# Kernel optimization log

Hardware: AMD Instinct MI355X
Metric: run time of the kernel (lower is better)

## Reference

```python
import jax, jax.numpy as jnp
import numpy as np

B, T, E, H = 4, 4096, 512, 64

def setup_inputs() -> dict:
    key = jax.random.key(0)
    k1, k2, k3, k4 = jax.random.split(key, 4)
    x = jax.random.normal(k1, (B, T, E), dtype=jnp.float32)
    # nn.Linear(E, H, bias=False) weight has shape [H, E]; y = x @ W.T
    Wq = jax.random.normal(k2, (H, E), dtype=jnp.float32) * (E ** -0.5)
    Wk = jax.random.normal(k3, (H, E), dtype=jnp.float32) * (E ** -0.5)
    Wv = jax.random.normal(k4, (H, E), dtype=jnp.float32) * (E ** -0.5)
    return {"x": x, "Wq": Wq, "Wk": Wk, "Wv": Wv}

def reference(x, Wq, Wk, Wv):
    # projections: [B, T, H]
    q = jnp.einsum('bte,he->bth', x, Wq)
    k = jnp.einsum('bte,he->bth', x, Wk)
    v = jnp.einsum('bte,he->bth', x, Wv)
    scale = 1.0 / jnp.sqrt(jnp.float32(q.shape[-1]))
    scores = jnp.einsum('bth,bsh->bts', q, k) * scale  # [B, T, T]
    t = scores.shape[-1]
    causal = jnp.tril(jnp.ones((t, t), dtype=bool))
    scores = jnp.where(causal, scores, -jnp.inf)
    probs = jax.nn.softmax(scores, axis=-1)
    # dropout p=0.0 (eval) -> identity
    return jnp.einsum('bts,bsh->bth', probs, v)
```

## Files before the change

kernel.cpp:

```cpp
#include <hip/hip_runtime.h>
#include <hip/hip_bf16.h>

#define Bn 4
#define Tn 4096
#define En 512
#define Hn 64
#define NEGINF -3e38f
#define QSCALE 0.1803368801f

typedef __attribute__((ext_vector_type(8))) __bf16 bf16x8;
typedef __attribute__((ext_vector_type(4))) __bf16 bf16x4;
typedef __attribute__((ext_vector_type(4))) float f32x4;

#define MFMA16(a, b, c) __builtin_amdgcn_mfma_f32_16x16x32_bf16(a, b, c, 0, 0, 0)

__device__ __forceinline__ float bf2f(unsigned short u) {
    union { unsigned u; float f; } v; v.u = ((unsigned)u) << 16;
    return v.f;
}
__device__ __forceinline__ unsigned cvtpk(float a, float b) {
    unsigned d;
    asm("v_cvt_pk_bf16_f32 %0, %1, %2" : "=v"(d) : "v"(a), "v"(b));
    return d;
}
__device__ __forceinline__ unsigned short f2bf(float f) {
    union { float f; unsigned u; } v; v.f = f;
    unsigned r = v.u + 0x7fffu + ((v.u >> 16) & 1u);
    return (unsigned short)(r >> 16);
}
__device__ __forceinline__ float exp2fast(float x) {
    float r;
    asm("v_exp_f32 %0, %1" : "=v"(r) : "v"(x));
    return r;
}
__device__ __forceinline__ void gl16(const void* g, void* l) {
    __builtin_amdgcn_global_load_lds(
        (const __attribute__((address_space(1))) unsigned int*)g,
        (__attribute__((address_space(3))) unsigned int*)l, 16, 0, 0);
}

__launch_bounds__(256, 2)
__global__ void proj(const float* __restrict__ x, const float* __restrict__ Wq,
                     const float* __restrict__ Wk, const float* __restrict__ Wv,
                     unsigned short* __restrict__ q16, unsigned short* __restrict__ k16,
                     unsigned short* __restrict__ vt16) {
    __shared__ __align__(16) unsigned char plds[2][28672];
    const int tid = threadIdx.x;
    const int w = tid >> 6, lane = tid & 63, r = lane & 15, g = lane >> 4;
    const int row0 = blockIdx.x * 32;
    const int rsel = (w & 1) * 16, csel = (w >> 1) * 96;

    const int srow = tid >> 3, skc = (tid & 7) * 8;
    const int sby = (tid & 7) * 16;

    f32x4 acc[6];
#pragma unroll
    for (int i = 0; i < 6; ++i) acc[i] = (f32x4){0.f, 0.f, 0.f, 0.f};

    {
        const float4* xp = (const float4*)&x[(row0 + srow) * En + skc];
        float4 f0 = xp[0], f1 = xp[1];
        union { bf16x8 v; unsigned u32[4]; } t;
        t.u32[0] = cvtpk(f0.x, f0.y); t.u32[1] = cvtpk(f0.z, f0.w);
        t.u32[2] = cvtpk(f1.x, f1.y); t.u32[3] = cvtpk(f1.z, f1.w);
        *(bf16x8*)&plds[0][srow * 128 + (sby ^ ((srow & 7) << 4))] = t.v;
#pragma unroll
        for (int c2 = 0; c2 < 6; ++c2) {
            const float* Ws = (c2 < 2) ? Wq : ((c2 < 4) ? Wk : Wv);
            int wr = (c2 & 1) * 32 + srow;
            const float4* wp = (const float4*)&Ws[wr * En + skc];
            float4 w0 = wp[0], w1 = wp[1];
            union { bf16x8 v; unsigned u32[4]; } tw;
            tw.u32[0] = cvtpk(w0.x, w0.y); tw.u32[1] = cvtpk(w0.z, w0.w);
            tw.u32[2] = cvtpk(w1.x, w1.y); tw.u32[3] = cvtpk(w1.z, w1.w);
            int wrow = c2 * 32 + srow;
            *(bf16x8*)&plds[0][4096 + wrow * 128 + (sby ^ ((wrow & 7) << 4))] = tw.v;
        }
    }
    __syncthreads();

    for (int s = 0; s < 8; ++s) {
        const int pp = s & 1;
        const bool more = (s < 7);
        float4 nf0, nf1;
        float4 nw0[6], nw1[6];
        if (more) {
            int k1 = (s + 1) * 64;
            const float4* xp = (const float4*)&x[(row0 + srow) * En + k1 + skc];
            nf0 = xp[0]; nf1 = xp[1];
#pragma unroll
            for (int c2 = 0; c2 < 6; ++c2) {
                const float* Ws = (c2 < 2) ? Wq : ((c2 < 4) ? Wk : Wv);
                int wr = (c2 & 1) * 32 + srow;
                const float4* wp = (const float4*)&Ws[wr * En + k1 + skc];
                nw0[c2] = wp[0]; nw1[c2] = wp[1];
            }
        }
        {
            const unsigned char* A = &plds[pp][0];
            const unsigned char* W = &plds[pp][4096];
            int arow = rsel + r, asw = (arow & 7) << 4;
            bf16x8 a0 = *(const bf16x8*)&A[arow * 128 + ((g * 16) ^ asw)];
            bf16x8 a1 = *(const bf16x8*)&A[arow * 128 + ((64 + g * 16) ^ asw)];
#pragma unroll
            for (int ct = 0; ct < 6; ++ct) {
                int wrow = csel + ct * 16 + r, wsw = (wrow & 7) << 4;
                bf16x8 b0 = *(const bf16x8*)&W[wrow * 128 + ((g * 16) ^ wsw)];
                bf16x8 b1 = *(const bf16x8*)&W[wrow * 128 + ((64 + g * 16) ^ wsw)];
                acc[ct] = MFMA16(a0, b0, acc[ct]);
                acc[ct] = MFMA16(a1, b1, acc[ct]);
            }
        }
        if (more) {
            unsigned char* D = &plds[pp ^ 1][0];
            union { bf16x8 v; unsigned u32[4]; } t;
            t.u32[0] = cvtpk(nf0.x, nf0.y); t.u32[1] = cvtpk(nf0.z, nf0.w);
            t.u32[2] = cvtpk(nf1.x, nf1.y); t.u32[3] = cvtpk(nf1.z, nf1.w);
            *(bf16x8*)&D[srow * 128 + (sby ^ ((srow & 7) << 4))] = t.v;
#pragma unroll
            for (int c2 = 0; c2 < 6; ++c2) {
                union { bf16x8 v; unsigned u32[4]; } tw;
                tw.u32[0] = cvtpk(nw0[c2].x, nw0[c2].y); tw.u32[1] = cvtpk(nw0[c2].z, nw0[c2].w);
                tw.u32[2] = cvtpk(nw1[c2].x, nw1[c2].y); tw.u32[3] = cvtpk(nw1[c2].z, nw1[c2].w);
                int wrow = c2 * 32 + srow;
                *(bf16x8*)&D[4096 + wrow * 128 + (sby ^ ((wrow & 7) << 4))] = tw.v;
            }
        }
        __syncthreads();
    }
#pragma unroll
    for (int ct = 0; ct < 6; ++ct) {
        int n = csel + ct * 16 + r;
#pragma unroll
        for (int reg = 0; reg < 4; ++reg) {
            int gr = row0 + rsel + g * 4 + reg;
            if (n < 64) {
                q16[gr * 64 + n] = f2bf(acc[ct][reg] * QSCALE);
            } else if (n < 128) {
                k16[gr * 64 + (n - 64)] = f2bf(acc[ct][reg]);
            } else {
                int h = n - 128; int bb = gr >> 12; int t = gr & 4095;
                vt16[((bb * 64 + h) << 12) + t] = f2bf(acc[ct][reg]);
            }
        }
    }
}

__launch_bounds__(256, 5)
__global__ void attnp(const unsigned short* __restrict__ q16, const unsigned short* __restrict__ k16,
                      const unsigned short* __restrict__ vt16,
                      unsigned short* __restrict__ po, float* __restrict__ lp) {
    __shared__ __align__(16) unsigned char lds[2][16384];

    const int tid = threadIdx.x;
    const int w = tid >> 6, lane = tid & 63, r = lane & 15, g = lane >> 4;
    const int bid = blockIdx.x;
    const int page = bid >> 8, idx = bid & 255;
    const int s5 = idx >> 3, b = (idx >> 1) & 3, q1 = idx & 1;
    int jt, piece, t0, tEnd;
    if (page < 3) {
        jt = 63 - s5;
        int nt = jt + 1;
        piece = page + 3 * q1;
        t0 = (piece * nt) / 6; tEnd = ((piece + 1) * nt) / 6;
    } else {
        jt = s5;
        int nt = jt + 1;
        piece = (page - 3) + 2 * q1;
        t0 = (piece * nt) / 4; tEnd = ((piece + 1) * nt) / 4;
    }
    const size_t kbase = (size_t)b * Tn;
    const int q0 = jt * 64;
    const int wq0 = q0 + w * 16;

    const unsigned short* Kb = k16 + kbase * 64;
    const unsigned short* Vb = vt16 + ((size_t)(b * 64) << 12);

    const int srl = lane >> 3, scb = (lane & 7) * 16;

    bf16x8 bq0, bq1;
    {
        const unsigned short* qp = &q16[(kbase + wq0 + r) * 64 + g * 8];
        bq0 = *(const bf16x8*)qp;
        bq1 = *(const bf16x8*)(qp + 32);
    }

    f32x4 o[4];
#pragma unroll
    for (int i = 0; i < 4; ++i) o[i] = (f32x4){0.f, 0.f, 0.f, 0.f};
    float l_ = 0.f;

    if (tEnd > t0) {
        int kv0 = t0 * 64;
#pragma unroll
        for (int i = 0; i < 4; ++i) {
            int cc = w * 4 + i;
            if (cc < 8) {
                int row = cc * 8 + srl, sw = (row & 7) << 4;
                gl16((const char*)Kb + (size_t)(kv0 + row) * 128 + (scb ^ sw),
                     &lds[0][cc * 1024]);
            } else {
                int h = (cc - 8) * 8 + srl, sw = (h & 7) << 4;
                gl16((const char*)Vb + (size_t)h * 8192 + (size_t)kv0 * 2 + (scb ^ sw),
                     &lds[0][cc * 1024]);
            }
        }
    }
    __syncthreads();

    int pp = 0;
    for (int it = t0; it < tEnd; ++it, pp ^= 1) {
        const bool more = (it + 1 < tEnd);
        if (more) {
            int nkv = (it + 1) * 64;
#pragma unroll
            for (int i = 0; i < 4; ++i) {
                int cc = w * 4 + i;
                if (cc < 8) {
                    int row = cc * 8 + srl, sw = (row & 7) << 4;
                    gl16((const char*)Kb + (size_t)(nkv + row) * 128 + (scb ^ sw),
                         &lds[pp ^ 1][cc * 1024]);
                } else {
                    int h = (cc - 8) * 8 + srl, sw = (h & 7) << 4;
                    gl16((const char*)Vb + (size_t)h * 8192 + (size_t)nkv * 2 + (scb ^ sw),
                         &lds[pp ^ 1][cc * 1024]);
                }
            }
        }
        const int kv0 = it * 64;
        if (kv0 <= wq0 + 15) {
            const unsigned char* K = &lds[pp][0];
            const unsigned char* V = &lds[pp][8192];
            f32x4 s4[4];
            __builtin_amdgcn_s_setprio(1);
#pragma unroll
            for (int ct = 0; ct < 4; ++ct) {
                int row = ct * 16 + r;
                int base = row * 128, sw = (row & 7) << 4;
                bf16x8 ak0 = *(const bf16x8*)&K[base + ((g * 16) ^ sw)];
                bf16x8 ak1 = *(const bf16x8*)&K[base + ((64 + g * 16) ^ sw)];
                f32x4 t = (f32x4){0.f, 0.f, 0.f, 0.f};
                t = MFMA16(ak0, bq0, t);
                t = MFMA16(ak1, bq1, t);
                s4[ct] = t;
            }
            __builtin_amdgcn_s_setprio(0);
            if (kv0 + 63 > wq0) {
                int qq = wq0 + r;
#pragma unroll
                for (int ct = 0; ct < 4; ++ct)
#pragma unroll
                    for (int reg = 0; reg < 4; ++reg) {
                        int kv = kv0 + ct * 16 + g * 4 + reg;
                        if (kv > qq) s4[ct][reg] = NEGINF;
                    }
            }
#pragma unroll
            for (int ct = 0; ct < 4; ++ct)
#pragma unroll
                for (int reg = 0; reg < 4; ++reg)
                    s4[ct][reg] = exp2fast(s4[ct][reg]);
            l_ += ((s4[0][0] + s4[0][1]) + (s4[0][2] + s4[0][3])) +
                  ((s4[1][0] + s4[1][1]) + (s4[1][2] + s4[1][3])) +
                  ((s4[2][0] + s4[2][1]) + (s4[2][2] + s4[2][3])) +
                  ((s4[3][0] + s4[3][1]) + (s4[3][2] + s4[3][3]));
            union { bf16x8 v; unsigned u32[4]; } pk[2];
#pragma unroll
            for (int kf = 0; kf < 2; ++kf) {
                pk[kf].u32[0] = cvtpk(s4[kf * 2][0], s4[kf * 2][1]);
                pk[kf].u32[1] = cvtpk(s4[kf * 2][2], s4[kf * 2][3]);
                pk[kf].u32[2] = cvtpk(s4[kf * 2 + 1][0], s4[kf * 2 + 1][1]);
                pk[kf].u32[3] = cvtpk(s4[kf * 2 + 1][2], s4[kf * 2 + 1][3]);
            }
            __builtin_amdgcn_s_setprio(1);
#pragma unroll
            for (int cth = 0; cth < 4; ++cth) {
                int h = cth * 16 + r;
                int vb = h * 128, sw2 = (h & 7) << 4;
#pragma unroll
                for (int kf = 0; kf < 2; ++kf) {
                    int off = kf * 64 + g * 8;
                    union { bf16x8 v; bf16x4 h4[2]; } vv;
                    vv.h4[0] = *(const bf16x4*)&V[vb + (off ^ sw2)];
                    vv.h4[1] = *(const bf16x4*)&V[vb + ((off + 32) ^ sw2)];
                    o[cth] = MFMA16(pk[kf].v, vv.v, o[cth]);
                }
            }
            __builtin_amdgcn_s_setprio(0);
        }
        __syncthreads();
    }

    const size_t qb = (size_t)piece * 16384 + b * 4096;
#pragma unroll
    for (int cth = 0; cth < 4; ++cth)
#pragma unroll
        for (int reg = 0; reg < 4; ++reg)
            po[(qb + wq0 + g * 4 + reg) * 64 + cth * 16 + r] = f2bf(o[cth][reg]);
    lp[(qb + wq0 + r) * 4 + g] = l_;
}

__global__ void merge(const unsigned short* __restrict__ po, const float* __restrict__ lp,
                      float* __restrict__ out) {
    int t = blockIdx.x * 256 + threadIdx.x;
    int q = t >> 3, c8 = (t & 7) * 8;
    int tloc = (q & 4095) >> 6;
    int ns = (tloc >= 32) ? 6 : 4;
    float L = 0.f;
    for (int c = 0; c < ns; ++c)
#pragma unroll
        for (int gg = 0; gg < 4; ++gg)
            L += lp[((size_t)c * 16384 + q) * 4 + gg];
    float inv = 1.0f / L;
    float acc[8] = {0.f, 0.f, 0.f, 0.f, 0.f, 0.f, 0.f, 0.f};
    for (int c = 0; c < ns; ++c) {
        union { uint4 v; unsigned short u[8]; } ld;
        ld.v = *(const uint4*)&po[((size_t)c * 16384 + q) * 64 + c8];
#pragma unroll
        for (int j = 0; j < 8; ++j) acc[j] += bf2f(ld.u[j]);
    }
    float4* op = (float4*)&out[(size_t)q * 64 + c8];
    op[0] = (float4){acc[0] * inv, acc[1] * inv, acc[2] * inv, acc[3] * inv};
    op[1] = (float4){acc[4] * inv, acc[5] * inv, acc[6] * inv, acc[7] * inv};
}

extern "C" void kernel_launch(void* const* d_in, const int* in_sizes, int n_in,
                              void* d_out, int out_size, void* d_ws, size_t ws_size,
                              hipStream_t stream) {
    const float* x  = (const float*)d_in[0];
    const float* Wq = (const float*)d_in[1];
    const float* Wk = (const float*)d_in[2];
    const float* Wv = (const float*)d_in[3];
    float* out = (float*)d_out;
    char* ws = (char*)d_ws;

    unsigned short* q16 = (unsigned short*)ws;
    unsigned short* k16 = (unsigned short*)(ws + 2097152);
    unsigned short* v16 = (unsigned short*)(ws + 4194304);
    unsigned short* po  = (unsigned short*)(ws + 6291456);
    float*          lp  = (float*)(ws + 18874368);

    hipLaunchKernelGGL(proj, dim3(512), dim3(256), 0, stream, x, Wq, Wk, Wv, q16, k16, v16);
    hipLaunchKernelGGL(attnp, dim3(1280), dim3(256), 0, stream, q16, k16, v16, po, lp);
    hipLaunchKernelGGL(merge, dim3(512), dim3(256), 0, stream, po, lp, out);
}
```

Before: 46.76 us.

## Split every query tile into four KV chunks and use one barrier per iteration

The attention work split changes from a mixed 6-way/4-way scheme (1280 blocks) to a uniform 4-way split over KV tiles (1024 blocks), pairing long and short query tiles by block index. The merge kernel then always combines four partials with unrolled loops. The pipeline drops the trailing __syncthreads and instead waits on vmcnt and issues one barrier at the top of each iteration, with buffer parity taken from the tile index. Launch bounds drop from 5 to 4 waves per SIMD. This may trade load balance across CUs for less merge work and fewer synchronisations.

```diff
diff --git a/kernel.cpp b/kernel.cpp
--- a/kernel.cpp
+++ b/kernel.cpp
@@ -146,7 +146,7 @@
     }
 }
 
-__launch_bounds__(256, 5)
+__launch_bounds__(256, 4)
 __global__ void attnp(const unsigned short* __restrict__ q16, const unsigned short* __restrict__ k16,
                       const unsigned short* __restrict__ vt16,
                       unsigned short* __restrict__ po, float* __restrict__ lp) {
@@ -155,22 +155,15 @@
     const int tid = threadIdx.x;
     const int w = tid >> 6, lane = tid & 63, r = lane & 15, g = lane >> 4;
     const int bid = blockIdx.x;
-    const int page = bid >> 8, idx = bid & 255;
+    const int k_ = bid >> 8, idx = bid & 255;
     const int s5 = idx >> 3, b = (idx >> 1) & 3, q1 = idx & 1;
-    int jt, piece, t0, tEnd;
-    if (page < 3) {
-        jt = 63 - s5;
-        int nt = jt + 1;
-        piece = page + 3 * q1;
-        t0 = (piece * nt) / 6; tEnd = ((piece + 1) * nt) / 6;
-    } else {
-        jt = s5;
-        int nt = jt + 1;
-        piece = (page - 3) + 2 * q1;
-        t0 = (piece * nt) / 4; tEnd = ((piece + 1) * nt) / 4;
-    }
+    const int jt = (k_ & 1) ? s5 : 63 - s5;
+    const int quarter = ((k_ >> 1) << 1) | q1;
     const size_t kbase = (size_t)b * Tn;
     const int q0 = jt * 64;
+    const int nt = jt + 1;
+    const int t0 = (quarter * nt) >> 2;
+    const int tEnd = ((quarter + 1) * nt) >> 2;
     const int wq0 = q0 + w * 16;
 
     const unsigned short* Kb = k16 + kbase * 64;
@@ -192,38 +185,37 @@
 
     if (tEnd > t0) {
         int kv0 = t0 * 64;
+        unsigned char* D = &lds[t0 & 1][0];
 #pragma unroll
         for (int i = 0; i < 4; ++i) {
             int cc = w * 4 + i;
             if (cc < 8) {
                 int row = cc * 8 + srl, sw = (row & 7) << 4;
-                gl16((const char*)Kb + (size_t)(kv0 + row) * 128 + (scb ^ sw),
-                     &lds[0][cc * 1024]);
+                gl16((const char*)Kb + (size_t)(kv0 + row) * 128 + (scb ^ sw), D + cc * 1024);
             } else {
                 int h = (cc - 8) * 8 + srl, sw = (h & 7) << 4;
-                gl16((const char*)Vb + (size_t)h * 8192 + (size_t)kv0 * 2 + (scb ^ sw),
-                     &lds[0][cc * 1024]);
-            }
-        }
-    }
-    __syncthreads();
-
-    int pp = 0;
-    for (int it = t0; it < tEnd; ++it, pp ^= 1) {
-        const bool more = (it + 1 < tEnd);
-        if (more) {
+                gl16((const char*)Vb + (size_t)h * 8192 + (size_t)kv0 * 2 + (scb ^ sw), D + cc * 1024);
+            }
+        }
+    }
+
+    for (int it = t0; it < tEnd; ++it) {
+        const int pp = it & 1;
+        asm volatile("s_waitcnt vmcnt(0)" ::: "memory");
+        __builtin_amdgcn_s_barrier();
+        __builtin_amdgcn_sched_barrier(0);
+        if (it + 1 < tEnd) {
             int nkv = (it + 1) * 64;
+            unsigned char* D = &lds[pp ^ 1][0];
 #pragma unroll
             for (int i = 0; i < 4; ++i) {
                 int cc = w * 4 + i;
                 if (cc < 8) {
                     int row = cc * 8 + srl, sw = (row & 7) << 4;
-                    gl16((const char*)Kb + (size_t)(nkv + row) * 128 + (scb ^ sw),
-                         &lds[pp ^ 1][cc * 1024]);
+                    gl16((const char*)Kb + (size_t)(nkv + row) * 128 + (scb ^ sw), D + cc * 1024);
                 } else {
                     int h = (cc - 8) * 8 + srl, sw = (h & 7) << 4;
-                    gl16((const char*)Vb + (size_t)h * 8192 + (size_t)nkv * 2 + (scb ^ sw),
-                         &lds[pp ^ 1][cc * 1024]);
+                    gl16((const char*)Vb + (size_t)h * 8192 + (size_t)nkv * 2 + (scb ^ sw), D + cc * 1024);
                 }
             }
         }
@@ -288,10 +280,9 @@
             }
             __builtin_amdgcn_s_setprio(0);
         }
-        __syncthreads();
-    }
-
-    const size_t qb = (size_t)piece * 16384 + b * 4096;
+    }
+
+    const size_t qb = (size_t)quarter * 16384 + b * 4096;
 #pragma unroll
     for (int cth = 0; cth < 4; ++cth)
 #pragma unroll
@@ -304,16 +295,16 @@
                       float* __restrict__ out) {
     int t = blockIdx.x * 256 + threadIdx.x;
     int q = t >> 3, c8 = (t & 7) * 8;
-    int tloc = (q & 4095) >> 6;
-    int ns = (tloc >= 32) ? 6 : 4;
     float L = 0.f;
-    for (int c = 0; c < ns; ++c)
+#pragma unroll
+    for (int c = 0; c < 4; ++c)
 #pragma unroll
         for (int gg = 0; gg < 4; ++gg)
             L += lp[((size_t)c * 16384 + q) * 4 + gg];
     float inv = 1.0f / L;
     float acc[8] = {0.f, 0.f, 0.f, 0.f, 0.f, 0.f, 0.f, 0.f};
-    for (int c = 0; c < ns; ++c) {
+#pragma unroll
+    for (int c = 0; c < 4; ++c) {
         union { uint4 v; unsigned short u[8]; } ld;
         ld.v = *(const uint4*)&po[((size_t)c * 16384 + q) * 64 + c8];
 #pragma unroll
@@ -338,9 +329,9 @@
     unsigned short* k16 = (unsigned short*)(ws + 2097152);
     unsigned short* v16 = (unsigned short*)(ws + 4194304);
     unsigned short* po  = (unsigned short*)(ws + 6291456);
-    float*          lp  = (float*)(ws + 18874368);
+    float*          lp  = (float*)(ws + 14680064);
 
     hipLaunchKernelGGL(proj, dim3(512), dim3(256), 0, stream, x, Wq, Wk, Wv, q16, k16, v16);
-    hipLaunchKernelGGL(attnp, dim3(1280), dim3(256), 0, stream, q16, k16, v16, po, lp);
+    hipLaunchKernelGGL(attnp, dim3(1024), dim3(256), 0, stream, q16, k16, v16, po, lp);
     hipLaunchKernelGGL(merge, dim3(512), dim3(256), 0, stream, po, lp, out);
 }
```

After: 44.38 us. 5.1% less time.
